# Performance work log

Measured on AMD Instinct MI355X. Metric: run time of the kernel, lower is better.

Reference implementation:

```python
import jax, jax.numpy as jnp
import numpy as np

N_NODES, N_EDGES, N_GRAPHS = 200000, 600000, 4000
IN_DIM, EDGE_DIM, HIDDEN, DEPTH = 25, 11, 128, 4
BN_EPS = 1e-5

def lrelu(x):
    return jnp.where(x > 0, x, 0.1 * x)

def setup_inputs() -> dict:
    key = jax.random.key(0)
    ks = jax.random.split(key, 8)
    x = jax.random.normal(ks[0], (N_NODES, IN_DIM), jnp.float32)
    edge_index = jax.random.randint(ks[1], (2, N_EDGES), 0, N_NODES, jnp.int32)
    edge_attr = jax.random.normal(ks[2], (N_EDGES, EDGE_DIM), jnp.float32)
    batch = jnp.sort(jax.random.randint(ks[3], (N_NODES,), 0, N_GRAPHS, jnp.int32))
    def init_w(k, shape, fan_in):
        return jax.random.normal(k, shape, jnp.float32) * np.float32(1.0 / np.sqrt(fan_in))
    W_in = init_w(ks[4], (IN_DIM, HIDDEN), IN_DIM)
    b_in = jnp.zeros((HIDDEN,), jnp.float32)
    W_msg = init_w(ks[5], (DEPTH, HIDDEN + EDGE_DIM, HIDDEN), HIDDEN + EDGE_DIM)
    b_msg = jnp.zeros((DEPTH, HIDDEN), jnp.float32)
    W_up = init_w(ks[6], (DEPTH, 2 * HIDDEN, HIDDEN), 2 * HIDDEN)
    b_up = jnp.zeros((DEPTH, HIDDEN), jnp.float32)
    gamma = jnp.ones((DEPTH, HIDDEN), jnp.float32)
    beta = jnp.zeros((DEPTH, HIDDEN), jnp.float32)
    return dict(x=x, edge_index=edge_index, edge_attr=edge_attr, batch=batch,
                W_in=W_in, b_in=b_in, W_msg=W_msg, b_msg=b_msg,
                W_up=W_up, b_up=b_up, gamma=gamma, beta=beta)

def reference(x, edge_index, edge_attr, batch, W_in, b_in, W_msg, b_msg, W_up, b_up, gamma, beta):
    N = x.shape[0]
    src, dst = edge_index[0], edge_index[1]  # PyG: x_j = x[src], aggregate at dst
    h = lrelu(x @ W_in + b_in)  # input_proj + leaky_relu(0.1)
    depth = W_msg.shape[0]
    for i in range(depth):
        # message: leaky_relu(Linear(cat[x_j, edge_attr]))
        msg = lrelu(jnp.concatenate([h[src], edge_attr], axis=-1) @ W_msg[i] + b_msg[i])
        aggr = jax.ops.segment_sum(msg, dst, num_segments=N)  # scatter-add
        # update: leaky_relu(Linear(cat[aggr, x]))
        out = lrelu(jnp.concatenate([aggr, h], axis=-1) @ W_up[i] + b_up[i])
        out = jax.nn.relu(out)
        # BatchNorm over node dim (training-mode batch statistics)
        mu = out.mean(axis=0)
        var = out.var(axis=0)
        h = gamma[i] * (out - mu) * jax.lax.rsqrt(var + BN_EPS) + beta[i]
        # dropout is identity at eval
    cnt = jax.ops.segment_sum(jnp.ones((N,), h.dtype), batch, num_segments=N_GRAPHS)
    summed = jax.ops.segment_sum(h, batch, num_segments=N_GRAPHS)
    return summed / jnp.maximum(cnt, 1.0)[:, None]  # global_mean_pool -> [G, H]
```

## Files before the change

kernel.cpp:

```cpp
#include <hip/hip_runtime.h>

#define N_NODES  200000
#define N_EDGES  600000
#define N_GRAPHS 4000
#define IN_DIM   25
#define EDGE_DIM 11
#define HIDDEN   128
#define DEPTH    4
#define BN_EPS   1e-5f

#define UB   32
#define NBLK (N_NODES / UB)
#define CHUNK  256
#define NCHUNK ((N_NODES + CHUNK - 1) / CHUNK)

typedef unsigned short ushortT;
typedef __attribute__((ext_vector_type(8))) short short8v;
typedef __attribute__((ext_vector_type(4))) float float4v;

__device__ __forceinline__ float lrelu(float v) { return v > 0.f ? v : 0.1f * v; }

__device__ __forceinline__ ushortT f2bf(float f) {
    unsigned u = __builtin_bit_cast(unsigned, f);
    u = (u + 0x7fffu + ((u >> 16) & 1u)) >> 16;
    return (ushortT)u;
}
__device__ __forceinline__ float bf2f(ushortT h) {
    unsigned u = ((unsigned)h) << 16;
    return __builtin_bit_cast(float, u);
}

__global__ void k_hist(const int* __restrict__ ei, int* __restrict__ cnt)
{
    const int e = blockIdx.x * 256 + threadIdx.x;
    if (e < N_EDGES) atomicAdd(&cnt[ei[N_EDGES + e]], 1);
}

__global__ __launch_bounds__(256) void k_chunk_sum(const int* __restrict__ cnt,
                                                   int* __restrict__ bsum)
{
    const int t = threadIdx.x;
    const int i = blockIdx.x * CHUNK + t;
    int v = (i < N_NODES) ? cnt[i] : 0;
    #pragma unroll
    for (int off = 32; off > 0; off >>= 1) v += __shfl_down(v, off);
    __shared__ int ws[4];
    if ((t & 63) == 0) ws[t >> 6] = v;
    __syncthreads();
    if (t == 0) bsum[blockIdx.x] = ws[0] + ws[1] + ws[2] + ws[3];
}

__global__ __launch_bounds__(1024) void k_scan_bsums(const int* __restrict__ bsum,
                                                     int* __restrict__ bscan)
{
    __shared__ int s[1024];
    const int t = threadIdx.x;
    const int v = (t < NCHUNK) ? bsum[t] : 0;
    s[t] = v; __syncthreads();
    for (int off = 1; off < 1024; off <<= 1) {
        const int x = (t >= off) ? s[t - off] : 0;
        __syncthreads();
        s[t] += x;
        __syncthreads();
    }
    if (t < NCHUNK) bscan[t] = s[t] - v;
}

__global__ __launch_bounds__(256) void k_chunk_scan(const int* __restrict__ cnt,
                                                    const int* __restrict__ bscan,
                                                    int* __restrict__ off_work)
{
    __shared__ int s[CHUNK];
    const int b = blockIdx.x, t = threadIdx.x;
    const int i = b * CHUNK + t;
    const int v = (i < N_NODES) ? cnt[i] : 0;
    s[t] = v; __syncthreads();
    for (int off = 1; off < CHUNK; off <<= 1) {
        const int x = (t >= off) ? s[t - off] : 0;
        __syncthreads();
        s[t] += x;
        __syncthreads();
    }
    if (i < N_NODES) off_work[i] = bscan[b] + s[t] - v;
}

__global__ void k_scatter(const int* __restrict__ ei, int* __restrict__ off_work,
                          int* __restrict__ srcS, int* __restrict__ dstS,
                          int* __restrict__ perm)
{
    const int e = blockIdx.x * 256 + threadIdx.x;
    if (e < N_EDGES) {
        const int d = ei[N_EDGES + e];
        const int pos = atomicAdd(&off_work[d], 1);
        srcS[pos] = ei[e];
        dstS[pos] = d;
        perm[pos] = e;
    }
}

__global__ __launch_bounds__(256) void k_prep_ea(const float* __restrict__ ea,
                                                 const int* __restrict__ perm,
                                                 ushortT* __restrict__ ea16)
{
    const size_t i = (size_t)blockIdx.x * 256 + threadIdx.x;
    if (i >= (size_t)N_EDGES * 16) return;
    const int e = (int)(i >> 4), c = (int)(i & 15);
    const int pe = perm[e];
    ea16[i] = (c < EDGE_DIM) ? f2bf(ea[(size_t)pe * EDGE_DIM + c]) : (ushortT)0;
}

__global__ __launch_bounds__(256) void k_prep_wmsg(const float* __restrict__ W,
                                                   ushortT* __restrict__ Wf)
{
    const int i = blockIdx.x * 256 + threadIdx.x;
    if (i >= DEPTH * 20480) return;
    const int d = i / 20480, r = i % 20480;
    const int j = r & 7, lane = (r >> 3) & 63, tile = r >> 9;
    const int ct = tile & 7, kt = tile >> 3;
    const int k = kt * 32 + ((lane >> 4) << 3) + j;
    const int c = ct * 16 + (lane & 15);
    Wf[i] = (k < HIDDEN + EDGE_DIM)
          ? f2bf(W[((size_t)d * (HIDDEN + EDGE_DIM) + k) * HIDDEN + c]) : (ushortT)0;
}

__global__ __launch_bounds__(256) void k_prep_wup(const float* __restrict__ W,
                                                  ushortT* __restrict__ Wf)
{
    const int i = blockIdx.x * 256 + threadIdx.x;
    if (i >= DEPTH * 32768) return;
    const int d = i / 32768, r = i % 32768;
    const int j = r & 7, lane = (r >> 3) & 63, tile = r >> 9;
    const int ct = tile & 7, kt = tile >> 3;
    const int k = kt * 32 + ((lane >> 4) << 3) + j;
    const int c = ct * 16 + (lane & 15);
    Wf[i] = f2bf(W[((size_t)d * 2 * HIDDEN + k) * HIDDEN + c]);
}

__global__ __launch_bounds__(128) void k_input_proj(const float* __restrict__ x,
                                                    const float* __restrict__ W,
                                                    const float* __restrict__ b,
                                                    ushortT* __restrict__ h16)
{
    const int t  = threadIdx.x;
    const int n0 = blockIdx.x * 8;
    __shared__ float sW[IN_DIM * HIDDEN];
    __shared__ float sx[8][IN_DIM];
    for (int i = t; i < IN_DIM * HIDDEN; i += 128) sW[i] = W[i];
    for (int i = t; i < 8 * IN_DIM; i += 128) {
        int n = i / IN_DIM, k = i % IN_DIM;
        sx[n][k] = x[(size_t)(n0 + n) * IN_DIM + k];
    }
    __syncthreads();
    const float bt = b[t];
    for (int n = 0; n < 8; ++n) {
        float acc = bt;
        #pragma unroll
        for (int k = 0; k < IN_DIM; ++k) acc += sx[n][k] * sW[k * HIDDEN + t];
        h16[(size_t)(n0 + n) * HIDDEN + t] = f2bf(lrelu(acc));
    }
}

__global__ __launch_bounds__(256) void k_edge_mfma(const ushortT* __restrict__ h16,
                                                   const int*     __restrict__ srcS,
                                                   const int*     __restrict__ dstS,
                                                   const ushortT* __restrict__ ea16,
                                                   const ushortT* __restrict__ Wf,
                                                   const float*   __restrict__ bmsg,
                                                   float*         __restrict__ aggr)
{
    const int t    = threadIdx.x;
    const int wave = t >> 6, lane = t & 63;
    const int e0   = blockIdx.x * 64;

    __shared__ __align__(16) unsigned char smem[64 * 132 * 4];
    ushortT (*sA)[168]   = reinterpret_cast<ushortT (*)[168]>(smem);
    float   (*sMsg)[132] = reinterpret_cast<float (*)[132]>(smem);
    __shared__ int sSrc[64];
    __shared__ int sDst[64];

    const int ct0 = wave * 2;
    short8v B[5][2];
    const short8v* wp = reinterpret_cast<const short8v*>(Wf);
    #pragma unroll
    for (int kt = 0; kt < 5; ++kt) {
        B[kt][0] = wp[(size_t)(kt * 8 + ct0) * 64 + lane];
        B[kt][1] = wp[(size_t)(kt * 8 + ct0 + 1) * 64 + lane];
    }

    if (t < 64) { sSrc[t] = srcS[e0 + t]; sDst[t] = dstS[e0 + t]; }
    __syncthreads();

    for (int i = t; i < 64 * 16; i += 256) {
        const int e = i >> 4, q = i & 15;
        const uint4 v = reinterpret_cast<const uint4*>(h16)[(size_t)sSrc[e] * 16 + q];
        *reinterpret_cast<uint4*>(&sA[e][q * 8]) = v;
    }
    for (int i = t; i < 64 * 2; i += 256) {
        const int e = i >> 1, q = i & 1;
        const uint4 v = reinterpret_cast<const uint4*>(ea16)[((size_t)(e0 + e)) * 2 + q];
        *reinterpret_cast<uint4*>(&sA[e][128 + q * 8]) = v;
    }
    if (t < 128) {
        const int e = t >> 1, q = t & 1;
        const uint4 z = {0u, 0u, 0u, 0u};
        *reinterpret_cast<uint4*>(&sA[e][144 + q * 8]) = z;
    }
    __syncthreads();

    float4v acc[4][2];
    #pragma unroll
    for (int m = 0; m < 4; ++m) { acc[m][0] = (float4v)(0.f); acc[m][1] = (float4v)(0.f); }

    const int kOff = (lane >> 4) * 8;
    #pragma unroll
    for (int m = 0; m < 4; ++m) {
        const int row = m * 16 + (lane & 15);
        #pragma unroll
        for (int kt = 0; kt < 5; ++kt) {
            const short8v a = *reinterpret_cast<const short8v*>(&sA[row][kt * 32 + kOff]);
            acc[m][0] = __builtin_amdgcn_mfma_f32_16x16x32_bf16(a, B[kt][0], acc[m][0], 0, 0, 0);
            acc[m][1] = __builtin_amdgcn_mfma_f32_16x16x32_bf16(a, B[kt][1], acc[m][1], 0, 0, 0);
        }
    }
    __syncthreads();

    const int col = lane & 15;
    const int r0  = (lane >> 4) * 4;
    #pragma unroll
    for (int c = 0; c < 2; ++c) {
        const int ccol = (ct0 + c) * 16 + col;
        const float bt = bmsg[ccol];
        #pragma unroll
        for (int m = 0; m < 4; ++m) {
            #pragma unroll
            for (int j = 0; j < 4; ++j) {
                sMsg[m * 16 + r0 + j][ccol] = lrelu(acc[m][c][j] + bt);
            }
        }
    }
    __syncthreads();

    const int half = t >> 7;
    const int c    = t & 127;
    const int base = half * 32;
    float a = 0.f;
    int cur = sDst[base];
    bool atStart = true;
    for (int e = base; e < base + 32; ++e) {
        const int d = sDst[e];
        if (d != cur) {
            if (atStart) atomicAdd(&aggr[(size_t)cur * HIDDEN + c], a);
            else         aggr[(size_t)cur * HIDDEN + c] = a;
            atStart = false; cur = d; a = 0.f;
        }
        a += sMsg[e][c];
    }
    atomicAdd(&aggr[(size_t)cur * HIDDEN + c], a);
}

__global__ __launch_bounds__(256) void k_update_mfma(float*         __restrict__ aggr,
                                                     const ushortT* __restrict__ h16,
                                                     const ushortT* __restrict__ Wf,
                                                     const float*   __restrict__ bup,
                                                     float*         __restrict__ p_sum,
                                                     float*         __restrict__ p_sumsq)
{
    const int t    = threadIdx.x;
    const int wave = t >> 6, lane = t & 63;
    const int n0   = blockIdx.x * UB;

    __shared__ __align__(16) ushortT sA[UB][264];
    __shared__ __align__(16) ushortT sLo[UB][136];

    const int ct0 = wave * 2;
    short8v Bh[8][2];
    const short8v* wp = reinterpret_cast<const short8v*>(Wf);
    #pragma unroll
    for (int kt = 0; kt < 8; ++kt) {
        Bh[kt][0] = wp[(size_t)(kt * 8 + ct0) * 64 + lane];
        Bh[kt][1] = wp[(size_t)(kt * 8 + ct0 + 1) * 64 + lane];
    }

    for (int i = t; i < UB * 32; i += 256) {
        const int n = i >> 5, q = i & 31;
        const float4 v = reinterpret_cast<const float4*>(aggr)[(size_t)(n0 + n) * 32 + q];
        union { ushortT s[4]; uint2 u; } hi, lo;
        #pragma unroll
        for (int j = 0; j < 4; ++j) {
            const float f = (&v.x)[j];
            const ushortT hb = f2bf(f);
            hi.s[j] = hb;
            lo.s[j] = f2bf(f - bf2f(hb));
        }
        *reinterpret_cast<uint2*>(&sA[n][q * 4])  = hi.u;
        *reinterpret_cast<uint2*>(&sLo[n][q * 4]) = lo.u;
    }
    for (int i = t; i < UB * 16; i += 256) {
        const int n = i >> 4, q = i & 15;
        const uint4 v = reinterpret_cast<const uint4*>(h16)[(size_t)(n0 + n) * 16 + q];
        *reinterpret_cast<uint4*>(&sA[n][128 + q * 8]) = v;
    }
    __syncthreads();

    float4v acc[2][2];
    #pragma unroll
    for (int m = 0; m < 2; ++m) { acc[m][0] = (float4v)(0.f); acc[m][1] = (float4v)(0.f); }

    const int kOff = (lane >> 4) * 8;
    #pragma unroll
    for (int m = 0; m < 2; ++m) {
        const int row = m * 16 + (lane & 15);
        #pragma unroll
        for (int kt = 0; kt < 8; ++kt) {
            const short8v a = *reinterpret_cast<const short8v*>(&sA[row][kt * 32 + kOff]);
            acc[m][0] = __builtin_amdgcn_mfma_f32_16x16x32_bf16(a, Bh[kt][0], acc[m][0], 0, 0, 0);
            acc[m][1] = __builtin_amdgcn_mfma_f32_16x16x32_bf16(a, Bh[kt][1], acc[m][1], 0, 0, 0);
        }
        #pragma unroll
        for (int kt = 0; kt < 4; ++kt) {
            const short8v a = *reinterpret_cast<const short8v*>(&sLo[row][kt * 32 + kOff]);
            acc[m][0] = __builtin_amdgcn_mfma_f32_16x16x32_bf16(a, Bh[kt][0], acc[m][0], 0, 0, 0);
            acc[m][1] = __builtin_amdgcn_mfma_f32_16x16x32_bf16(a, Bh[kt][1], acc[m][1], 0, 0, 0);
        }
    }

    const int col = lane & 15;
    const int r0  = (lane >> 4) * 4;
    #pragma unroll
    for (int c = 0; c < 2; ++c) {
        const int ccol = (ct0 + c) * 16 + col;
        const float bt = bup[ccol];
        float s = 0.f, q = 0.f;
        #pragma unroll
        for (int m = 0; m < 2; ++m) {
            #pragma unroll
            for (int j = 0; j < 4; ++j) {
                const float v = fmaxf(acc[m][c][j] + bt, 0.f);
                s += v; q += v * v;
                aggr[(size_t)(n0 + m * 16 + r0 + j) * HIDDEN + ccol] = v;
            }
        }
        s += __shfl_xor(s, 16); s += __shfl_xor(s, 32);
        q += __shfl_xor(q, 16); q += __shfl_xor(q, 32);
        if (lane < 16) {
            p_sum  [(size_t)ccol * NBLK + blockIdx.x] = s;
            p_sumsq[(size_t)ccol * NBLK + blockIdx.x] = q;
        }
    }
}

__global__ __launch_bounds__(256) void k_bn_reduce(const float* __restrict__ p_sum,
                                                   const float* __restrict__ p_sumsq,
                                                   const float* __restrict__ gamma,
                                                   const float* __restrict__ beta,
                                                   float* __restrict__ scale,
                                                   float* __restrict__ shift)
{
    const int c = blockIdx.x, t = threadIdx.x;
    float s = 0.f, q = 0.f;
    for (int i = t; i < NBLK; i += 256) {
        s += p_sum  [(size_t)c * NBLK + i];
        q += p_sumsq[(size_t)c * NBLK + i];
    }
    #pragma unroll
    for (int off = 32; off > 0; off >>= 1) {
        s += __shfl_down(s, off);
        q += __shfl_down(q, off);
    }
    __shared__ float ls[4], lq[4];
    const int w = t >> 6;
    if ((t & 63) == 0) { ls[w] = s; lq[w] = q; }
    __syncthreads();
    if (t == 0) {
        s = ls[0] + ls[1] + ls[2] + ls[3];
        q = lq[0] + lq[1] + lq[2] + lq[3];
        const float mu  = s * (1.f / N_NODES);
        const float var = q * (1.f / N_NODES) - mu * mu;
        const float sc  = gamma[c] * rsqrtf(var + BN_EPS);
        scale[c] = sc;
        shift[c] = beta[c] - mu * sc;
    }
}

__global__ __launch_bounds__(256) void k_bn_norm(float* __restrict__ buf,
                                                 const float* __restrict__ scale,
                                                 const float* __restrict__ shift,
                                                 ushortT* __restrict__ h16)
{
    const size_t i = (size_t)blockIdx.x * 256 + threadIdx.x;
    if (i >= (size_t)N_NODES * HIDDEN / 4) return;
    const float4 v = reinterpret_cast<const float4*>(buf)[i];
    const int c0 = (int)((i * 4) & (HIDDEN - 1));
    union { ushortT s[4]; uint2 u; } p;
    p.s[0] = f2bf(v.x * scale[c0 + 0] + shift[c0 + 0]);
    p.s[1] = f2bf(v.y * scale[c0 + 1] + shift[c0 + 1]);
    p.s[2] = f2bf(v.z * scale[c0 + 2] + shift[c0 + 2]);
    p.s[3] = f2bf(v.w * scale[c0 + 3] + shift[c0 + 3]);
    reinterpret_cast<uint2*>(h16)[i] = p.u;
    const float4 z = {0.f, 0.f, 0.f, 0.f};
    reinterpret_cast<float4*>(buf)[i] = z;
}

__global__ void k_pool_cnt(const int* __restrict__ batch, float* __restrict__ cnt)
{
    const int n = blockIdx.x * 256 + threadIdx.x;
    if (n < N_NODES) atomicAdd(&cnt[batch[n]], 1.0f);
}

__global__ __launch_bounds__(128) void k_pool_sum(const ushortT* __restrict__ h16,
                                                  const int* __restrict__ batch,
                                                  float* __restrict__ pool)
{
    const int t  = threadIdx.x;
    const int n0 = blockIdx.x * 16;
    __shared__ int sb[16];
    if (t < 16) sb[t] = batch[n0 + t];
    __syncthreads();
    int g = sb[0];
    float acc = 0.f;
    for (int j = 0; j < 16; ++j) {
        const float v = bf2f(h16[(size_t)(n0 + j) * HIDDEN + t]);
        if (sb[j] != g) {
            atomicAdd(&pool[(size_t)g * HIDDEN + t], acc);
            g = sb[j];
            acc = v;
        } else {
            acc += v;
        }
    }
    atomicAdd(&pool[(size_t)g * HIDDEN + t], acc);
}

__global__ void k_pool_div(const float* __restrict__ pool,
                           const float* __restrict__ cnt,
                           float* __restrict__ out)
{
    const int i = blockIdx.x * 256 + threadIdx.x;
    if (i < N_GRAPHS * HIDDEN) {
        const int g = i >> 7;
        out[i] = pool[i] / fmaxf(cnt[g], 1.0f);
    }
}

extern "C" void kernel_launch(void* const* d_in, const int* in_sizes, int n_in,
                              void* d_out, int out_size, void* d_ws, size_t ws_size,
                              hipStream_t stream)
{
    const float* x     = (const float*)d_in[0];
    const int*   ei    = (const int*)  d_in[1];
    const float* ea    = (const float*)d_in[2];
    const int*   batch = (const int*)  d_in[3];
    const float* W_in  = (const float*)d_in[4];
    const float* b_in  = (const float*)d_in[5];
    const float* W_msg = (const float*)d_in[6];
    const float* b_msg = (const float*)d_in[7];
    const float* W_up  = (const float*)d_in[8];
    const float* b_up  = (const float*)d_in[9];
    const float* gamma = (const float*)d_in[10];
    const float* beta  = (const float*)d_in[11];
    float* out = (float*)d_out;

    float*   aggr  = (float*)d_ws;
    ushortT* h16   = (ushortT*)(aggr + (size_t)N_NODES * HIDDEN);
    ushortT* ea16  = h16 + (size_t)N_NODES * HIDDEN;
    ushortT* wmsgf = ea16 + (size_t)N_EDGES * 16;
    ushortT* wupf  = wmsgf + DEPTH * 20480;
    float*   bn_scale = (float*)(wupf + DEPTH * 32768);
    float*   bn_shift = bn_scale + HIDDEN;
    float*   pool     = bn_shift + HIDDEN;
    float*   cnt      = pool + (size_t)N_GRAPHS * HIDDEN;
    float*   p_sum    = cnt + N_GRAPHS;
    float*   p_sumsq  = p_sum + (size_t)HIDDEN * NBLK;
    int*     ecnt     = (int*)(p_sumsq + (size_t)HIDDEN * NBLK);
    int*     off_work = ecnt + N_NODES;
    int*     bsum     = off_work + N_NODES;
    int*     bscan    = bsum + 1024;
    int*     srcS     = bscan + 1024;
    int*     dstS     = srcS + N_EDGES;
    int*     perm     = dstS + N_EDGES;

    hipMemsetAsync(ecnt, 0, N_NODES * sizeof(int), stream);
    k_hist<<<(N_EDGES + 255) / 256, 256, 0, stream>>>(ei, ecnt);
    k_chunk_sum<<<NCHUNK, 256, 0, stream>>>(ecnt, bsum);
    k_scan_bsums<<<1, 1024, 0, stream>>>(bsum, bscan);
    k_chunk_scan<<<NCHUNK, 256, 0, stream>>>(ecnt, bscan, off_work);
    k_scatter<<<(N_EDGES + 255) / 256, 256, 0, stream>>>(ei, off_work, srcS, dstS, perm);

    k_prep_ea<<<(N_EDGES * 16 + 255) / 256, 256, 0, stream>>>(ea, perm, ea16);
    k_prep_wmsg<<<(DEPTH * 20480 + 255) / 256, 256, 0, stream>>>(W_msg, wmsgf);
    k_prep_wup<<<(DEPTH * 32768 + 255) / 256, 256, 0, stream>>>(W_up, wupf);
    k_input_proj<<<N_NODES / 8, 128, 0, stream>>>(x, W_in, b_in, h16);

    hipMemsetAsync(aggr, 0, (size_t)N_NODES * HIDDEN * sizeof(float), stream);
    for (int d = 0; d < DEPTH; ++d) {
        k_edge_mfma<<<N_EDGES / 64, 256, 0, stream>>>(
            h16, srcS, dstS, ea16, wmsgf + (size_t)d * 20480,
            b_msg + (size_t)d * HIDDEN, aggr);
        k_update_mfma<<<N_NODES / UB, 256, 0, stream>>>(
            aggr, h16, wupf + (size_t)d * 32768, b_up + (size_t)d * HIDDEN,
            p_sum, p_sumsq);
        k_bn_reduce<<<HIDDEN, 256, 0, stream>>>(p_sum, p_sumsq,
                                                gamma + (size_t)d * HIDDEN,
                                                beta + (size_t)d * HIDDEN,
                                                bn_scale, bn_shift);
        k_bn_norm<<<(N_NODES * HIDDEN / 4 + 255) / 256, 256, 0, stream>>>(
            aggr, bn_scale, bn_shift, h16);
    }

    hipMemsetAsync(pool, 0, ((size_t)N_GRAPHS * HIDDEN + N_GRAPHS) * sizeof(float), stream);
    k_pool_cnt<<<(N_NODES + 255) / 256, 256, 0, stream>>>(batch, cnt);
    k_pool_sum<<<N_NODES / 16, 128, 0, stream>>>(h16, batch, pool);
    k_pool_div<<<(N_GRAPHS * HIDDEN + 255) / 256, 256, 0, stream>>>(pool, cnt, out);
}
```

Measured before the change: 937.0 us.

## Fold BatchNorm affine into next layer weights and drop normalization pass

Each layer's BatchNorm scale and shift are folded into the next layer's message and update weights and biases by a small per-layer fold kernel. The final affine is applied inside the pooling kernel. The update kernel now writes the raw activation directly as bf16 to a ping-pong buffer, which removes the separate full-tensor normalize-and-zero pass. The full aggregation memset is replaced by zeroing only the rows that are written by atomics or have zero in-degree. This cuts large fp32 read and write traffic per layer, at the cost of extra launches and of applying bf16 rounding before the affine.

```diff
diff --git a/kernel.cpp b/kernel.cpp
--- a/kernel.cpp
+++ b/kernel.cpp
@@ -11,6 +11,7 @@
 
 #define UB   32
 #define NBLK (N_NODES / UB)
+#define NEBLK (N_EDGES / 64)
 #define CHUNK  256
 #define NCHUNK ((N_NODES + CHUNK - 1) / CHUNK)
 
@@ -98,6 +99,41 @@
     }
 }
 
+__global__ void k_flag_ends(const int* __restrict__ dstS, int* __restrict__ flag)
+{
+    const int i = blockIdx.x * 256 + threadIdx.x;
+    if (i < NEBLK * 4) {
+        const int b = i >> 2, p = i & 3;
+        const int pos = (p == 0) ? 0 : (p == 1) ? 31 : (p == 2) ? 32 : 63;
+        flag[dstS[b * 64 + pos]] = 1;
+    }
+}
+
+__global__ void k_flag_zdeg(const int* __restrict__ ecnt, int* __restrict__ flag)
+{
+    const int n = blockIdx.x * 256 + threadIdx.x;
+    if (n < N_NODES && ecnt[n] == 0) flag[n] = 1;
+}
+
+__global__ void k_compact(const int* __restrict__ flag, int* __restrict__ zlist,
+                          int* __restrict__ zcount)
+{
+    const int n = blockIdx.x * 256 + threadIdx.x;
+    if (n < N_NODES && flag[n]) zlist[atomicAdd(zcount, 1)] = n;
+}
+
+__global__ __launch_bounds__(256) void k_zero_rows(const int* __restrict__ zlist,
+                                                   const int* __restrict__ zcount,
+                                                   float* __restrict__ aggr)
+{
+    const int total = zcount[0] * 32;
+    const float4 z = {0.f, 0.f, 0.f, 0.f};
+    for (int i = blockIdx.x * 256 + threadIdx.x; i < total; i += gridDim.x * 256) {
+        const int row = zlist[i >> 5], q = i & 31;
+        reinterpret_cast<float4*>(aggr)[(size_t)row * 32 + q] = z;
+    }
+}
+
 __global__ __launch_bounds__(256) void k_prep_ea(const float* __restrict__ ea,
                                                  const int* __restrict__ perm,
                                                  ushortT* __restrict__ ea16)
@@ -109,31 +145,56 @@
     ea16[i] = (c < EDGE_DIM) ? f2bf(ea[(size_t)pe * EDGE_DIM + c]) : (ushortT)0;
 }
 
-__global__ __launch_bounds__(256) void k_prep_wmsg(const float* __restrict__ W,
-                                                   ushortT* __restrict__ Wf)
-{
-    const int i = blockIdx.x * 256 + threadIdx.x;
-    if (i >= DEPTH * 20480) return;
-    const int d = i / 20480, r = i % 20480;
-    const int j = r & 7, lane = (r >> 3) & 63, tile = r >> 9;
-    const int ct = tile & 7, kt = tile >> 3;
-    const int k = kt * 32 + ((lane >> 4) << 3) + j;
-    const int c = ct * 16 + (lane & 15);
-    Wf[i] = (k < HIDDEN + EDGE_DIM)
-          ? f2bf(W[((size_t)d * (HIDDEN + EDGE_DIM) + k) * HIDDEN + c]) : (ushortT)0;
-}
-
-__global__ __launch_bounds__(256) void k_prep_wup(const float* __restrict__ W,
-                                                  ushortT* __restrict__ Wf)
-{
-    const int i = blockIdx.x * 256 + threadIdx.x;
-    if (i >= DEPTH * 32768) return;
-    const int d = i / 32768, r = i % 32768;
-    const int j = r & 7, lane = (r >> 3) & 63, tile = r >> 9;
-    const int ct = tile & 7, kt = tile >> 3;
-    const int k = kt * 32 + ((lane >> 4) << 3) + j;
-    const int c = ct * 16 + (lane & 15);
-    Wf[i] = f2bf(W[((size_t)d * 2 * HIDDEN + k) * HIDDEN + c]);
+__global__ __launch_bounds__(256) void k_fold(const float* __restrict__ Wm,
+                                              const float* __restrict__ bm,
+                                              const float* __restrict__ Wu,
+                                              const float* __restrict__ bu,
+                                              const float* __restrict__ scale,
+                                              const float* __restrict__ shift,
+                                              ushortT* __restrict__ WmF,
+                                              float*   __restrict__ bmF,
+                                              ushortT* __restrict__ WuF,
+                                              float*   __restrict__ buF)
+{
+    const int b = blockIdx.x, t = threadIdx.x;
+    if (b < 80) {
+        const int i = b * 256 + t;
+        const int j = i & 7, lane = (i >> 3) & 63, tile = i >> 9;
+        const int ct = tile & 7, kt = tile >> 3;
+        const int k = kt * 32 + ((lane >> 4) << 3) + j;
+        const int c = ct * 16 + (lane & 15);
+        float v = (k < HIDDEN + EDGE_DIM) ? Wm[k * HIDDEN + c] : 0.f;
+        if (k < HIDDEN) v *= scale[k];
+        WmF[i] = f2bf(v);
+    } else if (b < 208) {
+        const int i = (b - 80) * 256 + t;
+        const int j = i & 7, lane = (i >> 3) & 63, tile = i >> 9;
+        const int ct = tile & 7, kt = tile >> 3;
+        const int k = kt * 32 + ((lane >> 4) << 3) + j;
+        const int c = ct * 16 + (lane & 15);
+        float v = Wu[k * HIDDEN + c];
+        if (k >= HIDDEN) v *= scale[k - HIDDEN];
+        WuF[i] = f2bf(v);
+    } else if (b == 208) {
+        if (t < HIDDEN) {
+            float acc = bm[t];
+            for (int k = 0; k < HIDDEN; ++k) acc += shift[k] * Wm[k * HIDDEN + t];
+            bmF[t] = acc;
+        }
+    } else {
+        if (t < HIDDEN) {
+            float acc = bu[t];
+            for (int k = 0; k < HIDDEN; ++k) acc += shift[k] * Wu[(HIDDEN + k) * HIDDEN + t];
+            buF[t] = acc;
+        }
+    }
+}
+
+__global__ void k_init_affine(float* __restrict__ scale, float* __restrict__ shift)
+{
+    const int t = threadIdx.x;
+    scale[t] = 1.f;
+    shift[t] = 0.f;
 }
 
 __global__ __launch_bounds__(128) void k_input_proj(const float* __restrict__ x,
@@ -258,10 +319,11 @@
     atomicAdd(&aggr[(size_t)cur * HIDDEN + c], a);
 }
 
-__global__ __launch_bounds__(256) void k_update_mfma(float*         __restrict__ aggr,
+__global__ __launch_bounds__(256) void k_update_mfma(const float*   __restrict__ aggr,
                                                      const ushortT* __restrict__ h16,
                                                      const ushortT* __restrict__ Wf,
                                                      const float*   __restrict__ bup,
+                                                     ushortT*       __restrict__ hout,
                                                      float*         __restrict__ p_sum,
                                                      float*         __restrict__ p_sumsq)
 {
@@ -337,7 +399,7 @@
             for (int j = 0; j < 4; ++j) {
                 const float v = fmaxf(acc[m][c][j] + bt, 0.f);
                 s += v; q += v * v;
-                aggr[(size_t)(n0 + m * 16 + r0 + j) * HIDDEN + ccol] = v;
+                hout[(size_t)(n0 + m * 16 + r0 + j) * HIDDEN + ccol] = f2bf(v);
             }
         }
         s += __shfl_xor(s, 16); s += __shfl_xor(s, 32);
@@ -382,25 +444,6 @@
     }
 }
 
-__global__ __launch_bounds__(256) void k_bn_norm(float* __restrict__ buf,
-                                                 const float* __restrict__ scale,
-                                                 const float* __restrict__ shift,
-                                                 ushortT* __restrict__ h16)
-{
-    const size_t i = (size_t)blockIdx.x * 256 + threadIdx.x;
-    if (i >= (size_t)N_NODES * HIDDEN / 4) return;
-    const float4 v = reinterpret_cast<const float4*>(buf)[i];
-    const int c0 = (int)((i * 4) & (HIDDEN - 1));
-    union { ushortT s[4]; uint2 u; } p;
-    p.s[0] = f2bf(v.x * scale[c0 + 0] + shift[c0 + 0]);
-    p.s[1] = f2bf(v.y * scale[c0 + 1] + shift[c0 + 1]);
-    p.s[2] = f2bf(v.z * scale[c0 + 2] + shift[c0 + 2]);
-    p.s[3] = f2bf(v.w * scale[c0 + 3] + shift[c0 + 3]);
-    reinterpret_cast<uint2*>(h16)[i] = p.u;
-    const float4 z = {0.f, 0.f, 0.f, 0.f};
-    reinterpret_cast<float4*>(buf)[i] = z;
-}
-
 __global__ void k_pool_cnt(const int* __restrict__ batch, float* __restrict__ cnt)
 {
     const int n = blockIdx.x * 256 + threadIdx.x;
@@ -409,6 +452,8 @@
 
 __global__ __launch_bounds__(128) void k_pool_sum(const ushortT* __restrict__ h16,
                                                   const int* __restrict__ batch,
+                                                  const float* __restrict__ scale,
+                                                  const float* __restrict__ shift,
                                                   float* __restrict__ pool)
 {
     const int t  = threadIdx.x;
@@ -416,10 +461,11 @@
     __shared__ int sb[16];
     if (t < 16) sb[t] = batch[n0 + t];
     __syncthreads();
+    const float sc = scale[t], sh = shift[t];
     int g = sb[0];
     float acc = 0.f;
     for (int j = 0; j < 16; ++j) {
-        const float v = bf2f(h16[(size_t)(n0 + j) * HIDDEN + t]);
+        const float v = sc * bf2f(h16[(size_t)(n0 + j) * HIDDEN + t]) + sh;
         if (sb[j] != g) {
             atomicAdd(&pool[(size_t)g * HIDDEN + t], acc);
             g = sb[j];
@@ -461,11 +507,14 @@
     float* out = (float*)d_out;
 
     float*   aggr  = (float*)d_ws;
-    ushortT* h16   = (ushortT*)(aggr + (size_t)N_NODES * HIDDEN);
-    ushortT* ea16  = h16 + (size_t)N_NODES * HIDDEN;
-    ushortT* wmsgf = ea16 + (size_t)N_EDGES * 16;
-    ushortT* wupf  = wmsgf + DEPTH * 20480;
-    float*   bn_scale = (float*)(wupf + DEPTH * 32768);
+    ushortT* hA    = (ushortT*)(aggr + (size_t)N_NODES * HIDDEN);
+    ushortT* hB    = hA + (size_t)N_NODES * HIDDEN;
+    ushortT* ea16  = hB + (size_t)N_NODES * HIDDEN;
+    ushortT* wmsgfA = ea16 + (size_t)N_EDGES * 16;
+    ushortT* wupfA  = wmsgfA + 20480;
+    float*   biasM  = (float*)(wupfA + 32768);
+    float*   biasU  = biasM + HIDDEN;
+    float*   bn_scale = biasU + HIDDEN;
     float*   bn_shift = bn_scale + HIDDEN;
     float*   pool     = bn_shift + HIDDEN;
     float*   cnt      = pool + (size_t)N_GRAPHS * HIDDEN;
@@ -478,37 +527,47 @@
     int*     srcS     = bscan + 1024;
     int*     dstS     = srcS + N_EDGES;
     int*     perm     = dstS + N_EDGES;
+    int*     flag     = perm + N_EDGES;
+    int*     zlist    = flag + N_NODES;
+    int*     zcount   = zlist + N_NODES;
 
     hipMemsetAsync(ecnt, 0, N_NODES * sizeof(int), stream);
+    hipMemsetAsync(flag, 0, N_NODES * sizeof(int), stream);
+    hipMemsetAsync(zcount, 0, sizeof(int), stream);
     k_hist<<<(N_EDGES + 255) / 256, 256, 0, stream>>>(ei, ecnt);
     k_chunk_sum<<<NCHUNK, 256, 0, stream>>>(ecnt, bsum);
     k_scan_bsums<<<1, 1024, 0, stream>>>(bsum, bscan);
     k_chunk_scan<<<NCHUNK, 256, 0, stream>>>(ecnt, bscan, off_work);
     k_scatter<<<(N_EDGES + 255) / 256, 256, 0, stream>>>(ei, off_work, srcS, dstS, perm);
+    k_flag_ends<<<(NEBLK * 4 + 255) / 256, 256, 0, stream>>>(dstS, flag);
+    k_flag_zdeg<<<(N_NODES + 255) / 256, 256, 0, stream>>>(ecnt, flag);
+    k_compact<<<(N_NODES + 255) / 256, 256, 0, stream>>>(flag, zlist, zcount);
 
     k_prep_ea<<<(N_EDGES * 16 + 255) / 256, 256, 0, stream>>>(ea, perm, ea16);
-    k_prep_wmsg<<<(DEPTH * 20480 + 255) / 256, 256, 0, stream>>>(W_msg, wmsgf);
-    k_prep_wup<<<(DEPTH * 32768 + 255) / 256, 256, 0, stream>>>(W_up, wupf);
-    k_input_proj<<<N_NODES / 8, 128, 0, stream>>>(x, W_in, b_in, h16);
-
-    hipMemsetAsync(aggr, 0, (size_t)N_NODES * HIDDEN * sizeof(float), stream);
+    k_input_proj<<<N_NODES / 8, 128, 0, stream>>>(x, W_in, b_in, hA);
+    k_init_affine<<<1, 128, 0, stream>>>(bn_scale, bn_shift);
+
+    ushortT* hcur = hA;
+    ushortT* hnext = hB;
     for (int d = 0; d < DEPTH; ++d) {
+        k_fold<<<210, 256, 0, stream>>>(
+            W_msg + (size_t)d * (HIDDEN + EDGE_DIM) * HIDDEN, b_msg + (size_t)d * HIDDEN,
+            W_up + (size_t)d * 2 * HIDDEN * HIDDEN, b_up + (size_t)d * HIDDEN,
+            bn_scale, bn_shift, wmsgfA, biasM, wupfA, biasU);
+        k_zero_rows<<<1024, 256, 0, stream>>>(zlist, zcount, aggr);
         k_edge_mfma<<<N_EDGES / 64, 256, 0, stream>>>(
-            h16, srcS, dstS, ea16, wmsgf + (size_t)d * 20480,
-            b_msg + (size_t)d * HIDDEN, aggr);
+            hcur, srcS, dstS, ea16, wmsgfA, biasM, aggr);
         k_update_mfma<<<N_NODES / UB, 256, 0, stream>>>(
-            aggr, h16, wupf + (size_t)d * 32768, b_up + (size_t)d * HIDDEN,
-            p_sum, p_sumsq);
+            aggr, hcur, wupfA, biasU, hnext, p_sum, p_sumsq);
         k_bn_reduce<<<HIDDEN, 256, 0, stream>>>(p_sum, p_sumsq,
                                                 gamma + (size_t)d * HIDDEN,
                                                 beta + (size_t)d * HIDDEN,
                                                 bn_scale, bn_shift);
-        k_bn_norm<<<(N_NODES * HIDDEN / 4 + 255) / 256, 256, 0, stream>>>(
-            aggr, bn_scale, bn_shift, h16);
+        ushortT* tmp = hcur; hcur = hnext; hnext = tmp;
     }
 
     hipMemsetAsync(pool, 0, ((size_t)N_GRAPHS * HIDDEN + N_GRAPHS) * sizeof(float), stream);
     k_pool_cnt<<<(N_NODES + 255) / 256, 256, 0, stream>>>(batch, cnt);
-    k_pool_sum<<<N_NODES / 16, 128, 0, stream>>>(h16, batch, pool);
+    k_pool_sum<<<N_NODES / 16, 128, 0, stream>>>(hcur, batch, bn_scale, bn_shift, pool);
     k_pool_div<<<(N_GRAPHS * HIDDEN + 255) / 256, 256, 0, stream>>>(pool, cnt, out);
 }
```

Result: faster. 883.4 us (-5.7%).
